# Kernel tuning notes

Hardware: AMD Instinct MI355X
Metric: run time of the kernel (lower is better)

## Reference

```python
import collections
import functools
import itertools
import math
import jax
import jax.numpy as jnp
import numpy as np

# Weight space: RNN-like {W_ih:(784,512), W_hh:(512,512), b:(512,)}, channels last.
N0, N1, C_IN, C_OUT = 784, 512, 16, 16
PERM_SPEC = [[0, 1], [1, 1], [1]]  # perm-group label per dim of each leaf
N_TERMS = [11, 25, 9]  # equivariant basis terms per output leaf (Bell-number products)


def diagonal_slice(X, matching_dims):
    out = jnp.diagonal(X, axis1=matching_dims[0], axis2=matching_dims[1])
    for dim in matching_dims[2:]:
        out = jnp.diagonal(out, axis1=dim, axis2=-1)
    return out


def find_missing_indices(lstA, lstB):
    setB = set(lstB)
    return [i for i, el in enumerate(lstA) if el not in setB]


def get_repeated_idcs(lst):
    index_map = {}
    for index, item in enumerate(lst):
        index_map.setdefault(item, []).append(index)
    return [idcs for idcs in index_map.values() if len(idcs) > 1]


def match_dim_order(X, X_idcs, out_idcs):
    X_idcs_copy = X_idcs[:]
    perm = []
    for idx in out_idcs:
        if idx in X_idcs_copy:
            i = X_idcs_copy.index(idx)
            perm.append(i)
            X_idcs_copy[i] = None
    X = jnp.transpose(X, perm)
    return X, [X_idcs[i] for i in perm]


def remove_idcs(lst, idcs):
    return [l for i, l in enumerate(lst) if i not in idcs]


def move_dims_to_end(X, dims):
    new_in_order = remove_idcs(list(range(X.ndim)), dims) + dims
    return jnp.transpose(X, new_in_order)


def generate_partitions(items):
    if len(items) == 1:
        yield [items]
        return
    first = items[0]
    for subpart in generate_partitions(items[1:]):
        for n, subset in enumerate(subpart):
            yield subpart[:n] + [[first] + subset] + subpart[n + 1:]
        yield [[first]] + subpart


def valid_partitions(indices, perms):
    groups = collections.defaultdict(list)
    for index, perm in zip(indices, perms):
        groups[perm].append(index)
    parts_per_group = [list(generate_partitions(g)) for g in groups.values()]
    for p in itertools.product(*parts_per_group):
        yield [s for s in itertools.chain(*p)]


def gen_terms(out_spec, in_spec, out_shape, inp):
    """Basis terms of an equivariant linear map from in_spec to out_spec."""
    terms = []
    k1, k2 = len(out_spec), len(in_spec)
    for partition in valid_partitions(list(range(k1 + k2)), list(out_spec) + list(in_spec)):
        indices = [-1] * (k1 + k2)
        for subset_idx, subset in enumerate(partition):
            for dim in subset:
                indices[dim] = subset_idx
        out_indices, in_indices = indices[:k1], indices[k1:]
        term = inp
        # Collapse repeated input indices via diagonals.
        while (rep_idcs := get_repeated_idcs(in_indices)):
            term = diagonal_slice(term, rep_idcs[0])
            idx = in_indices[rep_idcs[0][0]]
            in_indices = remove_idcs(in_indices, rep_idcs[0])
            in_indices.append(idx)
        # Mean-reduce input dims that do not appear in the output.
        agg_idcs = find_missing_indices(in_indices, out_indices)
        term = jnp.mean(term, axis=agg_idcs)
        in_indices = remove_idcs(in_indices, agg_idcs)
        # Scatter onto diagonals for repeated output indices.
        for diag_set in get_repeated_idcs(out_indices):
            dim_size, out_idx = out_shape[diag_set[0]], out_indices[diag_set[0]]
            matching_in_dims = [i for i, idx in enumerate(in_indices) if idx == out_idx]
            num_new_dims = len(diag_set) - len(matching_in_dims)
            term = move_dims_to_end(term, matching_in_dims)
            new_term = jnp.zeros(term.shape + (dim_size,) * num_new_dims, dtype=term.dtype)
            diag_slice = (jnp.s_[:],) * (new_term.ndim - len(diag_set)) + (jnp.arange(dim_size),) * len(diag_set)
            if not matching_in_dims:
                term = jnp.expand_dims(term, axis=-1)
            term = new_term.at[diag_slice].add(term)
            in_indices = remove_idcs(in_indices, matching_in_dims)
            in_indices.extend([out_idx] * len(diag_set))
        term, in_indices = match_dim_order(term, in_indices, out_indices)
        term = jnp.expand_dims(term, axis=find_missing_indices(out_indices, in_indices))
        terms.append(term)
    return terms


def setup_inputs() -> dict:
    key = jax.random.key(0)
    ks = jax.random.split(key, 6)
    inp = {
        "w_ih": jax.random.normal(ks[0], (N0, N1, C_IN), jnp.float32),
        "w_hh": jax.random.normal(ks[1], (N1, N1, C_IN), jnp.float32),
        "b": jax.random.normal(ks[2], (N1, C_IN), jnp.float32),
    }
    for i, n in enumerate(N_TERMS):
        scale = math.sqrt(2.0 / (C_IN * n))  # 'he' init, fan_in = c_in * n_terms
        inp[f"theta_{i}"] = scale * jax.random.normal(ks[3 + i], (n, C_IN, C_OUT), jnp.float32)
        inp[f"bias_{i}"] = jnp.zeros((C_OUT,), jnp.float32)
    return inp


def reference(w_ih, w_hh, b, theta_0, theta_1, theta_2, bias_0, bias_1, bias_2):
    flat_params = [w_ih, w_hh, b]
    thetas = [theta_0, theta_1, theta_2]
    biases = [bias_0, bias_1, bias_2]
    outs = []
    for i in range(3):
        terms_i = []
        for j in range(3):
            gen = jax.vmap(
                functools.partial(gen_terms, PERM_SPEC[i], PERM_SPEC[j], flat_params[i].shape),
                in_axes=-1, out_axes=-1)
            terms_i.extend(gen(flat_params[j]))
        out = biases[i]
        for k, term in enumerate(terms_i):
            out = out + term @ thetas[i][k]  # [..., c_in] @ [c_in, c_out]
        outs.append(out)
    return tuple(outs)
```

## Files before the change

### kernel.cpp

```cpp
#include <hip/hip_runtime.h>


#define N0 784
#define N1 512

__device__ __forceinline__ float4 f4add(float4 a, float4 b) {
  a.x += b.x; a.y += b.y; a.z += b.z; a.w += b.w; return a;
}

__global__ __launch_bounds__(256)
void k_stage1(const float* __restrict__ wih, const float* __restrict__ whh,
              float* __restrict__ rm_ih, float* __restrict__ cm_ih,
              float* __restrict__ rm_hh, float* __restrict__ cm_hh,
              float* __restrict__ d_hh) {
  __shared__ float4 red[256];
  int t = threadIdx.x, blk = blockIdx.x;
  float4 acc = make_float4(0.f, 0.f, 0.f, 0.f);
  float scale;
  float* dst;
  if (blk < N0) {
    const float4* row = (const float4*)(wih + (size_t)blk * 8192);
    for (int j = t; j < 2048; j += 256) acc = f4add(acc, row[j]);
    scale = 1.f / 512.f; dst = rm_ih + blk * 16;
  } else if (blk < N0 + N1) {
    int b = blk - N0, q = t & 3, g = t >> 2;
    for (int a = g; a < N0; a += 64)
      acc = f4add(acc, *(const float4*)(wih + (size_t)a * 8192 + b * 16 + q * 4));
    scale = 1.f / 784.f; dst = cm_ih + b * 16;
  } else if (blk < N0 + 2 * N1) {
    int b = blk - N0 - N1;
    const float4* row = (const float4*)(whh + (size_t)b * 8192);
    for (int j = t; j < 2048; j += 256) acc = f4add(acc, row[j]);
    scale = 1.f / 512.f; dst = rm_hh + b * 16;
  } else {
    int b = blk - N0 - 2 * N1, q = t & 3, g = t >> 2;
    for (int a = g; a < N1; a += 64)
      acc = f4add(acc, *(const float4*)(whh + (size_t)a * 8192 + b * 16 + q * 4));
    scale = 1.f / 512.f; dst = cm_hh + b * 16;
    if (t < 4) ((float4*)(d_hh + b * 16))[t] = *(const float4*)(whh + (size_t)b * 8192 + b * 16 + t * 4);
  }
  red[t] = acc; __syncthreads();
  #pragma unroll
  for (int s = 128; s >= 4; s >>= 1) {
    if (t < s) red[t] = f4add(red[t], red[t + s]);
    __syncthreads();
  }
  if (t < 4) {
    float4 m = red[t];
    ((float4*)dst)[t] = make_float4(m.x * scale, m.y * scale, m.z * scale, m.w * scale);
  }
}

__global__ __launch_bounds__(256)
void k_vec(const float* __restrict__ rm_ih, const float* __restrict__ cm_ih,
           const float* __restrict__ rm_hh, const float* __restrict__ cm_hh,
           const float* __restrict__ d_hh, const float* __restrict__ bvec,
           const float* __restrict__ th0, const float* __restrict__ bias0,
           const float* __restrict__ th1, const float* __restrict__ bias1,
           const float* __restrict__ th2, const float* __restrict__ bias2,
           float* __restrict__ A0C, float* __restrict__ B0,
           float* __restrict__ A1C, float* __restrict__ B1,
           float* __restrict__ DD1, float* __restrict__ out2) {
  __shared__ float th[11520];
  __shared__ float4 red[256];
  __shared__ float gv[4][16];
  __shared__ float sc[64];
  int t = threadIdx.x;
  {
    float4* t4 = (float4*)th;
    const float4* s0 = (const float4*)th0;
    const float4* s1 = (const float4*)th1;
    const float4* s2 = (const float4*)th2;
    for (int j = t; j < 704; j += 256) t4[j] = s0[j];
    for (int j = t; j < 1600; j += 256) t4[704 + j] = s1[j];
    for (int j = t; j < 576; j += 256) t4[2304 + j] = s2[j];
  }
  int q = t & 3, g = t >> 2;
  {
    float4 acc = make_float4(0.f, 0.f, 0.f, 0.f);
    for (int a = g; a < N0; a += 64) acc = f4add(acc, ((const float4*)rm_ih)[a * 4 + q]);
    red[t] = acc; __syncthreads();
    #pragma unroll
    for (int s = 128; s >= 4; s >>= 1) { if (t < s) red[t] = f4add(red[t], red[t + s]); __syncthreads(); }
    if (t < 4) {
      float4 m = red[t];
      gv[0][t * 4 + 0] = m.x / 784.f; gv[0][t * 4 + 1] = m.y / 784.f;
      gv[0][t * 4 + 2] = m.z / 784.f; gv[0][t * 4 + 3] = m.w / 784.f;
    }
    __syncthreads();
  }
  const float* srcs[3] = { d_hh, rm_hh, bvec };
  #pragma unroll
  for (int v = 0; v < 3; v++) {
    float4 acc = make_float4(0.f, 0.f, 0.f, 0.f);
    for (int a = g; a < N1; a += 64) acc = f4add(acc, ((const float4*)srcs[v])[a * 4 + q]);
    red[t] = acc; __syncthreads();
    #pragma unroll
    for (int s = 128; s >= 4; s >>= 1) { if (t < s) red[t] = f4add(red[t], red[t + s]); __syncthreads(); }
    if (t < 4) {
      float4 m = red[t];
      gv[v + 1][t * 4 + 0] = m.x / 512.f; gv[v + 1][t * 4 + 1] = m.y / 512.f;
      gv[v + 1][t * 4 + 2] = m.z / 512.f; gv[v + 1][t * 4 + 3] = m.w / 512.f;
    }
    __syncthreads();
  }
  {
    int co = t & 15, j = t >> 4, o = j * 16 + co;
    float g0v = gv[0][j], dm = gv[1][j], gh = gv[2][j], mv = gv[3][j];
    float4 p;
    p.x = g0v * th[768 + o]         + dm * th[1280 + o]        + gh * th[2048 + o]        + mv * th[2560 + o];
    p.y = g0v * th[2816 + 1024 + o] + dm * th[2816 + 2304 + o] + gh * th[2816 + 4864 + o] + mv * th[2816 + 6144 + o];
    p.z = g0v * th[2816 + 512 + o]  + dm * th[2816 + 1792 + o] + gh * th[2816 + 4096 + o] + mv * th[2816 + 5632 + o];
    p.w = g0v * th[9216 + 256 + o]  + dm * th[9216 + 768 + o]  + gh * th[9216 + 1536 + o] + mv * th[9216 + 2048 + o];
    red[t] = p; __syncthreads();
    #pragma unroll
    for (int s = 128; s >= 16; s >>= 1) { if (t < s) red[t] = f4add(red[t], red[t + s]); __syncthreads(); }
    if (t < 16) {
      float4 a = red[t];
      sc[t] = a.x + bias0[t];
      sc[16 + t] = a.y + bias1[t];
      sc[32 + t] = a.z;
      sc[48 + t] = a.w + bias2[t];
    }
    __syncthreads();
  }
  int idx = blockIdx.x * 256 + t;
  int i = idx >> 4, co = idx & 15;
  float a0 = sc[co];
  {
    const float4* r4 = (const float4*)(rm_ih + i * 16);
    #pragma unroll
    for (int kq = 0; kq < 4; kq++) {
      float4 r = r4[kq];
      float vr[4] = { r.x, r.y, r.z, r.w };
      #pragma unroll
      for (int e = 0; e < 4; e++) a0 += vr[e] * th[256 + (kq * 4 + e) * 16 + co];
    }
  }
  A0C[idx] = a0;
  if (i < N1) {
    float b0a = 0.f, a1 = sc[16 + co], b1a = 0.f, dd = sc[32 + co], o2 = sc[48 + co];
    const float4* c4 = (const float4*)(cm_ih + i * 16);
    const float4* d4 = (const float4*)(d_hh + i * 16);
    const float4* r4 = (const float4*)(rm_hh + i * 16);
    const float4* m4 = (const float4*)(cm_hh + i * 16);
    const float4* v4 = (const float4*)(bvec + i * 16);
    #pragma unroll
    for (int kq = 0; kq < 4; kq++) {
      float4 cq = c4[kq], dq = d4[kq], rq = r4[kq], mq = m4[kq], vq = v4[kq];
      float vc[4] = { cq.x, cq.y, cq.z, cq.w };
      float vd[4] = { dq.x, dq.y, dq.z, dq.w };
      float vr[4] = { rq.x, rq.y, rq.z, rq.w };
      float vm[4] = { mq.x, mq.y, mq.z, mq.w };
      float vb[4] = { vq.x, vq.y, vq.z, vq.w };
      #pragma unroll
      for (int e = 0; e < 4; e++) {
        int o = (kq * 4 + e) * 16 + co;
        float cmi = vc[e], d = vd[e], r = vr[e], cm = vm[e], v = vb[e];
        b0a += cmi * th[512 + o]         + d * th[1024 + o]        + r * th[1536 + o]        + cm * th[1792 + o]        + v * th[2304 + o];
        a1  += cmi * th[2816 + 768 + o]  + d * th[2816 + 2048 + o] + r * th[2816 + 4352 + o] + cm * th[2816 + 4608 + o] + v * th[2816 + 5888 + o];
        b1a += cmi * th[2816 + 256 + o]  + d * th[2816 + 1536 + o] + r * th[2816 + 3072 + o] + cm * th[2816 + 3840 + o] + v * th[2816 + 5376 + o];
        dd  += cmi * th[2816 + 0 + o]    + d * th[2816 + 1280 + o] + r * th[2816 + 2560 + o] + cm * th[2816 + 3584 + o] + v * th[2816 + 5120 + o];
        o2  += cmi * th[9216 + 0 + o]    + d * th[9216 + 512 + o]  + r * th[9216 + 1024 + o] + cm * th[9216 + 1280 + o] + v * th[9216 + 1792 + o];
      }
    }
    B0[idx] = b0a; A1C[idx] = a1; B1[idx] = b1a; DD1[idx] = dd; out2[idx] = o2;
  }
}

__global__ __launch_bounds__(256)
void k_out(const float* __restrict__ wih, const float* __restrict__ whh,
           const float* __restrict__ th0, const float* __restrict__ th1,
           const float* __restrict__ A0C, const float* __restrict__ B0,
           const float* __restrict__ A1C, const float* __restrict__ B1,
           const float* __restrict__ DD1,
           float* __restrict__ out0, float* __restrict__ out1) {
  if (blockIdx.x < 1024) {
    int tid = blockIdx.x * 256 + threadIdx.x;
    int q = tid & 3;
    int slot = tid >> 2;
    const int nslots = (1024 * 256) >> 2;
    float4 tq[16];
    #pragma unroll
    for (int k = 0; k < 16; k++) tq[k] = *(const float4*)(th0 + k * 16 + q * 4);
    for (int p = slot; p < N0 * N1; p += nslots) {
      const float4* row = (const float4*)(wih + (size_t)p * 16);
      float4 r0 = row[0], r1 = row[1], r2 = row[2], r3 = row[3];
      int a = p >> 9, bb = p & 511;
      float4 acc = *(const float4*)(A0C + a * 16 + q * 4);
      float4 b4 = *(const float4*)(B0 + bb * 16 + q * 4);
      acc.x += b4.x; acc.y += b4.y; acc.z += b4.z; acc.w += b4.w;
      float wv[16] = { r0.x, r0.y, r0.z, r0.w, r1.x, r1.y, r1.z, r1.w,
                       r2.x, r2.y, r2.z, r2.w, r3.x, r3.y, r3.z, r3.w };
      #pragma unroll
      for (int k = 0; k < 16; k++) {
        acc.x += wv[k] * tq[k].x; acc.y += wv[k] * tq[k].y;
        acc.z += wv[k] * tq[k].z; acc.w += wv[k] * tq[k].w;
      }
      *(float4*)(out0 + (size_t)p * 16 + q * 4) = acc;
    }
  } else {
    int tid = (blockIdx.x - 1024) * 256 + threadIdx.x;
    int q = tid & 7;
    int slot = tid >> 3;
    const int nslots = (1024 * 256) >> 3;
    float2 tA[16], tB[16];
    #pragma unroll
    for (int k = 0; k < 16; k++) {
      tA[k] = *(const float2*)(th1 + 13 * 256 + k * 16 + q * 2);
      tB[k] = *(const float2*)(th1 + 11 * 256 + k * 16 + q * 2);
    }
    for (int p = slot; p < N1 * N1; p += nslots) {
      int a = p >> 9, b = p & 511;
      const float4* ra = (const float4*)(whh + (size_t)p * 16);
      const float4* rt = (const float4*)(whh + (size_t)((b << 9) | a) * 16);
      float4 a0 = ra[0], a1v = ra[1], a2 = ra[2], a3 = ra[3];
      float4 t0 = rt[0], t1v = rt[1], t2 = rt[2], t3 = rt[3];
      float2 acc = *(const float2*)(A1C + a * 16 + q * 2);
      float2 bb = *(const float2*)(B1 + b * 16 + q * 2);
      acc.x += bb.x; acc.y += bb.y;
      if (a == b) {
        float2 dd = *(const float2*)(DD1 + a * 16 + q * 2);
        acc.x += dd.x; acc.y += dd.y;
      }
      float ya[16] = { a0.x, a0.y, a0.z, a0.w, a1v.x, a1v.y, a1v.z, a1v.w,
                       a2.x, a2.y, a2.z, a2.w, a3.x, a3.y, a3.z, a3.w };
      float yt[16] = { t0.x, t0.y, t0.z, t0.w, t1v.x, t1v.y, t1v.z, t1v.w,
                       t2.x, t2.y, t2.z, t2.w, t3.x, t3.y, t3.z, t3.w };
      #pragma unroll
      for (int k = 0; k < 16; k++) {
        acc.x += ya[k] * tA[k].x + yt[k] * tB[k].x;
        acc.y += ya[k] * tA[k].y + yt[k] * tB[k].y;
      }
      *(float2*)(out1 + (size_t)p * 16 + q * 2) = acc;
    }
  }
}

extern "C" void kernel_launch(void* const* d_in, const int* in_sizes, int n_in,
                              void* d_out, int out_size, void* d_ws, size_t ws_size,
                              hipStream_t stream) {
  const float* w_ih = (const float*)d_in[0];
  const float* w_hh = (const float*)d_in[1];
  const float* bvec = (const float*)d_in[2];
  const float *th0, *bias0, *th1, *bias1, *th2, *bias2;
  if (n_in >= 9 && in_sizes[4] == 16) {
    th0 = (const float*)d_in[3]; bias0 = (const float*)d_in[4];
    th1 = (const float*)d_in[5]; bias1 = (const float*)d_in[6];
    th2 = (const float*)d_in[7]; bias2 = (const float*)d_in[8];
  } else {
    th0 = (const float*)d_in[3]; th1 = (const float*)d_in[4]; th2 = (const float*)d_in[5];
    bias0 = (const float*)d_in[6]; bias1 = (const float*)d_in[7]; bias2 = (const float*)d_in[8];
  }
  float* ws    = (float*)d_ws;
  float* rm_ih = ws;
  float* cm_ih = rm_ih + 12544;
  float* rm_hh = cm_ih + 8192;
  float* cm_hh = rm_hh + 8192;
  float* d_hh  = cm_hh + 8192;
  float* A0C   = d_hh + 8192;
  float* B0    = A0C + 12544;
  float* A1C   = B0 + 8192;
  float* B1    = A1C + 8192;
  float* DD1   = B1 + 8192;
  float* out0 = (float*)d_out;
  float* out1 = out0 + (size_t)N0 * N1 * 16;
  float* out2 = out1 + (size_t)N1 * N1 * 16;

  hipLaunchKernelGGL(k_stage1, dim3(N0 + 3 * N1), dim3(256), 0, stream,
                     w_ih, w_hh, rm_ih, cm_ih, rm_hh, cm_hh, d_hh);
  hipLaunchKernelGGL(k_vec, dim3(49), dim3(256), 0, stream,
                     rm_ih, cm_ih, rm_hh, cm_hh, d_hh, bvec,
                     th0, bias0, th1, bias1, th2, bias2,
                     A0C, B0, A1C, B1, DD1, out2);
  hipLaunchKernelGGL(k_out, dim3(2048), dim3(256), 0, stream,
                     w_ih, w_hh, th0, th1, A0C, B0, A1C, B1, DD1, out0, out1);
}
```

Baseline: 153.6 us.

## Compute row and column means in one pass with per-block column partials

Stage 1 previously read each weight matrix twice: once per row for row means and once with strided column reads for column means. Now each block reads 4 rows once, accumulating row sums and per-block column partial sums in shared memory, and writes the partials to workspace. k_vec then reduces those partials to get the column means. This halves the stage-1 reads of the large weights, at the cost of extra partial writes and a serial 196/128-step reduction loop inside the small 49-block k_vec.

```diff
diff --git a/kernel.cpp b/kernel.cpp
--- a/kernel.cpp
+++ b/kernel.cpp
@@ -3,6 +3,9 @@
 
 #define N0 784
 #define N1 512
+#define RPB 4
+#define NB_IH (N0 / RPB)
+#define NB_HH (N1 / RPB)
 
 __device__ __forceinline__ float4 f4add(float4 a, float4 b) {
   a.x += b.x; a.y += b.y; a.z += b.z; a.w += b.w; return a;
@@ -10,51 +13,58 @@
 
 __global__ __launch_bounds__(256)
 void k_stage1(const float* __restrict__ wih, const float* __restrict__ whh,
-              float* __restrict__ rm_ih, float* __restrict__ cm_ih,
-              float* __restrict__ rm_hh, float* __restrict__ cm_hh,
-              float* __restrict__ d_hh) {
-  __shared__ float4 red[256];
+              float* __restrict__ rm_ih, float* __restrict__ rm_hh,
+              float* __restrict__ d_hh,
+              float* __restrict__ part_ih, float* __restrict__ part_hh) {
+  __shared__ float4 colacc[2048];
+  __shared__ float4 redAll[RPB][256];
   int t = threadIdx.x, blk = blockIdx.x;
-  float4 acc = make_float4(0.f, 0.f, 0.f, 0.f);
-  float scale;
-  float* dst;
-  if (blk < N0) {
-    const float4* row = (const float4*)(wih + (size_t)blk * 8192);
-    for (int j = t; j < 2048; j += 256) acc = f4add(acc, row[j]);
-    scale = 1.f / 512.f; dst = rm_ih + blk * 16;
-  } else if (blk < N0 + N1) {
-    int b = blk - N0, q = t & 3, g = t >> 2;
-    for (int a = g; a < N0; a += 64)
-      acc = f4add(acc, *(const float4*)(wih + (size_t)a * 8192 + b * 16 + q * 4));
-    scale = 1.f / 784.f; dst = cm_ih + b * 16;
-  } else if (blk < N0 + 2 * N1) {
-    int b = blk - N0 - N1;
-    const float4* row = (const float4*)(whh + (size_t)b * 8192);
-    for (int j = t; j < 2048; j += 256) acc = f4add(acc, row[j]);
-    scale = 1.f / 512.f; dst = rm_hh + b * 16;
-  } else {
-    int b = blk - N0 - 2 * N1, q = t & 3, g = t >> 2;
-    for (int a = g; a < N1; a += 64)
-      acc = f4add(acc, *(const float4*)(whh + (size_t)a * 8192 + b * 16 + q * 4));
-    scale = 1.f / 512.f; dst = cm_hh + b * 16;
-    if (t < 4) ((float4*)(d_hh + b * 16))[t] = *(const float4*)(whh + (size_t)b * 8192 + b * 16 + t * 4);
-  }
-  red[t] = acc; __syncthreads();
+  bool is_hh = blk >= NB_IH;
+  const float* W = is_hh ? whh : wih;
+  float* rm      = is_hh ? rm_hh : rm_ih;
+  float* part    = is_hh ? part_hh : part_ih;
+  int pblk = is_hh ? blk - NB_IH : blk;
+  int r0 = pblk * RPB;
+
+  for (int j = t; j < 2048; j += 256) colacc[j] = make_float4(0.f, 0.f, 0.f, 0.f);
+  #pragma unroll
+  for (int r = 0; r < RPB; r++) {
+    const float4* row = (const float4*)(W + (size_t)(r0 + r) * 8192);
+    float4 acc = make_float4(0.f, 0.f, 0.f, 0.f);
+    for (int j = t; j < 2048; j += 256) {
+      float4 v = row[j];
+      colacc[j] = f4add(colacc[j], v);
+      acc = f4add(acc, v);
+    }
+    redAll[r][t] = acc;
+  }
+  __syncthreads();
   #pragma unroll
   for (int s = 128; s >= 4; s >>= 1) {
-    if (t < s) red[t] = f4add(red[t], red[t + s]);
+    if (t < s) {
+      #pragma unroll
+      for (int r = 0; r < RPB; r++) redAll[r][t] = f4add(redAll[r][t], redAll[r][t + s]);
+    }
     __syncthreads();
   }
-  if (t < 4) {
-    float4 m = red[t];
-    ((float4*)dst)[t] = make_float4(m.x * scale, m.y * scale, m.z * scale, m.w * scale);
-  }
+  if (t < 16) {
+    int r = t >> 2, q = t & 3;
+    float4 m = redAll[r][q];
+    const float s = 1.f / 512.f;
+    ((float4*)(rm + (r0 + r) * 16))[q] = make_float4(m.x * s, m.y * s, m.z * s, m.w * s);
+  }
+  if (is_hh && t < 64) {
+    int r = t >> 4, ci = t & 15;
+    d_hh[(r0 + r) * 16 + ci] = whh[(size_t)(r0 + r) * 8192 + (r0 + r) * 16 + ci];
+  }
+  float4* p4 = (float4*)(part + (size_t)pblk * 8192);
+  for (int j = t; j < 2048; j += 256) p4[j] = colacc[j];
 }
 
 __global__ __launch_bounds__(256)
-void k_vec(const float* __restrict__ rm_ih, const float* __restrict__ cm_ih,
-           const float* __restrict__ rm_hh, const float* __restrict__ cm_hh,
+void k_vec(const float* __restrict__ rm_ih, const float* __restrict__ rm_hh,
            const float* __restrict__ d_hh, const float* __restrict__ bvec,
+           const float* __restrict__ part_ih, const float* __restrict__ part_hh,
            const float* __restrict__ th0, const float* __restrict__ bias0,
            const float* __restrict__ th1, const float* __restrict__ bias1,
            const float* __restrict__ th2, const float* __restrict__ bias2,
@@ -65,6 +75,8 @@
   __shared__ float4 red[256];
   __shared__ float gv[4][16];
   __shared__ float sc[64];
+  __shared__ float cmih_s[16][16];
+  __shared__ float cmhh_s[16][16];
   int t = threadIdx.x;
   {
     float4* t4 = (float4*)th;
@@ -75,6 +87,19 @@
     for (int j = t; j < 1600; j += 256) t4[704 + j] = s1[j];
     for (int j = t; j < 576; j += 256) t4[2304 + j] = s2[j];
   }
+  int il = t >> 4, co = t & 15;
+  int i0 = blockIdx.x * 16;
+  if (i0 < N1) {
+    int col = i0 + il;
+    float s1 = 0.f;
+    #pragma unroll 4
+    for (int p = 0; p < NB_IH; p++) s1 += part_ih[(size_t)p * 8192 + col * 16 + co];
+    cmih_s[il][co] = s1 * (1.f / 784.f);
+    float s2 = 0.f;
+    #pragma unroll 4
+    for (int p = 0; p < NB_HH; p++) s2 += part_hh[(size_t)p * 8192 + col * 16 + co];
+    cmhh_s[il][co] = s2 * (1.f / 512.f);
+  }
   int q = t & 3, g = t >> 2;
   {
     float4 acc = make_float4(0.f, 0.f, 0.f, 0.f);
@@ -105,7 +130,7 @@
     __syncthreads();
   }
   {
-    int co = t & 15, j = t >> 4, o = j * 16 + co;
+    int j = t >> 4, o = j * 16 + co;
     float g0v = gv[0][j], dm = gv[1][j], gh = gv[2][j], mv = gv[3][j];
     float4 p;
     p.x = g0v * th[768 + o]         + dm * th[1280 + o]        + gh * th[2048 + o]        + mv * th[2560 + o];
@@ -125,7 +150,7 @@
     __syncthreads();
   }
   int idx = blockIdx.x * 256 + t;
-  int i = idx >> 4, co = idx & 15;
+  int i = i0 + il;
   float a0 = sc[co];
   {
     const float4* r4 = (const float4*)(rm_ih + i * 16);
@@ -140,23 +165,21 @@
   A0C[idx] = a0;
   if (i < N1) {
     float b0a = 0.f, a1 = sc[16 + co], b1a = 0.f, dd = sc[32 + co], o2 = sc[48 + co];
-    const float4* c4 = (const float4*)(cm_ih + i * 16);
     const float4* d4 = (const float4*)(d_hh + i * 16);
     const float4* r4 = (const float4*)(rm_hh + i * 16);
-    const float4* m4 = (const float4*)(cm_hh + i * 16);
     const float4* v4 = (const float4*)(bvec + i * 16);
     #pragma unroll
     for (int kq = 0; kq < 4; kq++) {
-      float4 cq = c4[kq], dq = d4[kq], rq = r4[kq], mq = m4[kq], vq = v4[kq];
-      float vc[4] = { cq.x, cq.y, cq.z, cq.w };
+      float4 dq = d4[kq], rq = r4[kq], vq = v4[kq];
       float vd[4] = { dq.x, dq.y, dq.z, dq.w };
       float vr[4] = { rq.x, rq.y, rq.z, rq.w };
-      float vm[4] = { mq.x, mq.y, mq.z, mq.w };
       float vb[4] = { vq.x, vq.y, vq.z, vq.w };
       #pragma unroll
       for (int e = 0; e < 4; e++) {
-        int o = (kq * 4 + e) * 16 + co;
-        float cmi = vc[e], d = vd[e], r = vr[e], cm = vm[e], v = vb[e];
+        int k = kq * 4 + e;
+        int o = k * 16 + co;
+        float cmi = cmih_s[il][k], cm = cmhh_s[il][k];
+        float d = vd[e], r = vr[e], v = vb[e];
         b0a += cmi * th[512 + o]         + d * th[1024 + o]        + r * th[1536 + o]        + cm * th[1792 + o]        + v * th[2304 + o];
         a1  += cmi * th[2816 + 768 + o]  + d * th[2816 + 2048 + o] + r * th[2816 + 4352 + o] + cm * th[2816 + 4608 + o] + v * th[2816 + 5888 + o];
         b1a += cmi * th[2816 + 256 + o]  + d * th[2816 + 1536 + o] + r * th[2816 + 3072 + o] + cm * th[2816 + 3840 + o] + v * th[2816 + 5376 + o];
@@ -252,25 +275,25 @@
     th0 = (const float*)d_in[3]; th1 = (const float*)d_in[4]; th2 = (const float*)d_in[5];
     bias0 = (const float*)d_in[6]; bias1 = (const float*)d_in[7]; bias2 = (const float*)d_in[8];
   }
-  float* ws    = (float*)d_ws;
-  float* rm_ih = ws;
-  float* cm_ih = rm_ih + 12544;
-  float* rm_hh = cm_ih + 8192;
-  float* cm_hh = rm_hh + 8192;
-  float* d_hh  = cm_hh + 8192;
-  float* A0C   = d_hh + 8192;
-  float* B0    = A0C + 12544;
-  float* A1C   = B0 + 8192;
-  float* B1    = A1C + 8192;
-  float* DD1   = B1 + 8192;
+  float* ws      = (float*)d_ws;
+  float* rm_ih   = ws;
+  float* rm_hh   = rm_ih + 12544;
+  float* d_hh    = rm_hh + 8192;
+  float* A0C     = d_hh + 8192;
+  float* B0      = A0C + 12544;
+  float* A1C     = B0 + 8192;
+  float* B1      = A1C + 8192;
+  float* DD1     = B1 + 8192;
+  float* part_ih = DD1 + 8192;
+  float* part_hh = part_ih + NB_IH * 8192;
   float* out0 = (float*)d_out;
   float* out1 = out0 + (size_t)N0 * N1 * 16;
   float* out2 = out1 + (size_t)N1 * N1 * 16;
 
-  hipLaunchKernelGGL(k_stage1, dim3(N0 + 3 * N1), dim3(256), 0, stream,
-                     w_ih, w_hh, rm_ih, cm_ih, rm_hh, cm_hh, d_hh);
+  hipLaunchKernelGGL(k_stage1, dim3(NB_IH + NB_HH), dim3(256), 0, stream,
+                     w_ih, w_hh, rm_ih, rm_hh, d_hh, part_ih, part_hh);
   hipLaunchKernelGGL(k_vec, dim3(49), dim3(256), 0, stream,
-                     rm_ih, cm_ih, rm_hh, cm_hh, d_hh, bvec,
+                     rm_ih, rm_hh, d_hh, bvec, part_ih, part_hh,
                      th0, bias0, th1, bias1, th2, bias2,
                      A0C, B0, A1C, B1, DD1, out2);
   hipLaunchKernelGGL(k_out, dim3(2048), dim3(256), 0, stream,
```

New measurement: 170.8 us. +11.2%, slower.

## Hoist global means into a separate kernel and use nontemporal output stores

Applied to the files above, without the earlier changes.

The four global mean reductions move out of each of the 49 k_vec blocks into a new 4-block kernel, so they are no longer recomputed redundantly per block. The per-block scalar-coefficient reduction becomes a per-thread 16-step loop. The large output writes in k_out now use nontemporal stores to reduce cache pollution on a streaming write. This adds one more kernel launch and a small global buffer.

```diff
diff --git a/kernel.cpp b/kernel.cpp
--- a/kernel.cpp
+++ b/kernel.cpp
@@ -4,8 +4,19 @@
 #define N0 784
 #define N1 512
 
+typedef float v4f __attribute__((ext_vector_type(4)));
+typedef float v2f __attribute__((ext_vector_type(2)));
+
 __device__ __forceinline__ float4 f4add(float4 a, float4 b) {
   a.x += b.x; a.y += b.y; a.z += b.z; a.w += b.w; return a;
+}
+__device__ __forceinline__ void nt_store4(float* p, float4 v) {
+  v4f x; x[0] = v.x; x[1] = v.y; x[2] = v.z; x[3] = v.w;
+  __builtin_nontemporal_store(x, (v4f*)p);
+}
+__device__ __forceinline__ void nt_store2(float* p, float x0, float x1) {
+  v2f x; x[0] = x0; x[1] = x1;
+  __builtin_nontemporal_store(x, (v2f*)p);
 }
 
 __global__ __launch_bounds__(256)
@@ -52,9 +63,38 @@
 }
 
 __global__ __launch_bounds__(256)
+void k_small(const float* __restrict__ rm_ih, const float* __restrict__ d_hh,
+             const float* __restrict__ rm_hh, const float* __restrict__ bvec,
+             float* __restrict__ gv_g) {
+  __shared__ float4 red[256];
+  int t = threadIdx.x, q = t & 3, g = t >> 2;
+  const float* src; int n; float scale;
+  switch (blockIdx.x) {
+    case 0: src = rm_ih; n = N0; scale = 1.f / 784.f; break;
+    case 1: src = d_hh;  n = N1; scale = 1.f / 512.f; break;
+    case 2: src = rm_hh; n = N1; scale = 1.f / 512.f; break;
+    default: src = bvec; n = N1; scale = 1.f / 512.f; break;
+  }
+  float4 acc = make_float4(0.f, 0.f, 0.f, 0.f);
+  for (int a = g; a < n; a += 64) acc = f4add(acc, ((const float4*)src)[a * 4 + q]);
+  red[t] = acc; __syncthreads();
+  #pragma unroll
+  for (int s = 128; s >= 4; s >>= 1) {
+    if (t < s) red[t] = f4add(red[t], red[t + s]);
+    __syncthreads();
+  }
+  if (t < 4) {
+    float4 m = red[t];
+    float* dst = gv_g + blockIdx.x * 16 + t * 4;
+    dst[0] = m.x * scale; dst[1] = m.y * scale; dst[2] = m.z * scale; dst[3] = m.w * scale;
+  }
+}
+
+__global__ __launch_bounds__(256)
 void k_vec(const float* __restrict__ rm_ih, const float* __restrict__ cm_ih,
            const float* __restrict__ rm_hh, const float* __restrict__ cm_hh,
            const float* __restrict__ d_hh, const float* __restrict__ bvec,
+           const float* __restrict__ gv_g,
            const float* __restrict__ th0, const float* __restrict__ bias0,
            const float* __restrict__ th1, const float* __restrict__ bias1,
            const float* __restrict__ th2, const float* __restrict__ bias2,
@@ -62,9 +102,7 @@
            float* __restrict__ A1C, float* __restrict__ B1,
            float* __restrict__ DD1, float* __restrict__ out2) {
   __shared__ float th[11520];
-  __shared__ float4 red[256];
-  __shared__ float gv[4][16];
-  __shared__ float sc[64];
+  __shared__ float gvs[64];
   int t = threadIdx.x;
   {
     float4* t4 = (float4*)th;
@@ -74,59 +112,23 @@
     for (int j = t; j < 704; j += 256) t4[j] = s0[j];
     for (int j = t; j < 1600; j += 256) t4[704 + j] = s1[j];
     for (int j = t; j < 576; j += 256) t4[2304 + j] = s2[j];
-  }
-  int q = t & 3, g = t >> 2;
-  {
-    float4 acc = make_float4(0.f, 0.f, 0.f, 0.f);
-    for (int a = g; a < N0; a += 64) acc = f4add(acc, ((const float4*)rm_ih)[a * 4 + q]);
-    red[t] = acc; __syncthreads();
-    #pragma unroll
-    for (int s = 128; s >= 4; s >>= 1) { if (t < s) red[t] = f4add(red[t], red[t + s]); __syncthreads(); }
-    if (t < 4) {
-      float4 m = red[t];
-      gv[0][t * 4 + 0] = m.x / 784.f; gv[0][t * 4 + 1] = m.y / 784.f;
-      gv[0][t * 4 + 2] = m.z / 784.f; gv[0][t * 4 + 3] = m.w / 784.f;
-    }
-    __syncthreads();
-  }
-  const float* srcs[3] = { d_hh, rm_hh, bvec };
+    if (t < 64) gvs[t] = gv_g[t];
+  }
+  __syncthreads();
+  int co = t & 15;
+  float c0 = bias0[co], c1 = bias1[co], e1 = 0.f, s2v = bias2[co];
   #pragma unroll
-  for (int v = 0; v < 3; v++) {
-    float4 acc = make_float4(0.f, 0.f, 0.f, 0.f);
-    for (int a = g; a < N1; a += 64) acc = f4add(acc, ((const float4*)srcs[v])[a * 4 + q]);
-    red[t] = acc; __syncthreads();
-    #pragma unroll
-    for (int s = 128; s >= 4; s >>= 1) { if (t < s) red[t] = f4add(red[t], red[t + s]); __syncthreads(); }
-    if (t < 4) {
-      float4 m = red[t];
-      gv[v + 1][t * 4 + 0] = m.x / 512.f; gv[v + 1][t * 4 + 1] = m.y / 512.f;
-      gv[v + 1][t * 4 + 2] = m.z / 512.f; gv[v + 1][t * 4 + 3] = m.w / 512.f;
-    }
-    __syncthreads();
-  }
-  {
-    int co = t & 15, j = t >> 4, o = j * 16 + co;
-    float g0v = gv[0][j], dm = gv[1][j], gh = gv[2][j], mv = gv[3][j];
-    float4 p;
-    p.x = g0v * th[768 + o]         + dm * th[1280 + o]        + gh * th[2048 + o]        + mv * th[2560 + o];
-    p.y = g0v * th[2816 + 1024 + o] + dm * th[2816 + 2304 + o] + gh * th[2816 + 4864 + o] + mv * th[2816 + 6144 + o];
-    p.z = g0v * th[2816 + 512 + o]  + dm * th[2816 + 1792 + o] + gh * th[2816 + 4096 + o] + mv * th[2816 + 5632 + o];
-    p.w = g0v * th[9216 + 256 + o]  + dm * th[9216 + 768 + o]  + gh * th[9216 + 1536 + o] + mv * th[9216 + 2048 + o];
-    red[t] = p; __syncthreads();
-    #pragma unroll
-    for (int s = 128; s >= 16; s >>= 1) { if (t < s) red[t] = f4add(red[t], red[t + s]); __syncthreads(); }
-    if (t < 16) {
-      float4 a = red[t];
-      sc[t] = a.x + bias0[t];
-      sc[16 + t] = a.y + bias1[t];
-      sc[32 + t] = a.z;
-      sc[48 + t] = a.w + bias2[t];
-    }
-    __syncthreads();
+  for (int j = 0; j < 16; j++) {
+    int o = j * 16 + co;
+    float g0v = gvs[j], dm = gvs[16 + j], gh = gvs[32 + j], mv = gvs[48 + j];
+    c0  += g0v * th[768 + o]         + dm * th[1280 + o]        + gh * th[2048 + o]        + mv * th[2560 + o];
+    c1  += g0v * th[2816 + 1024 + o] + dm * th[2816 + 2304 + o] + gh * th[2816 + 4864 + o] + mv * th[2816 + 6144 + o];
+    e1  += g0v * th[2816 + 512 + o]  + dm * th[2816 + 1792 + o] + gh * th[2816 + 4096 + o] + mv * th[2816 + 5632 + o];
+    s2v += g0v * th[9216 + 256 + o]  + dm * th[9216 + 768 + o]  + gh * th[9216 + 1536 + o] + mv * th[9216 + 2048 + o];
   }
   int idx = blockIdx.x * 256 + t;
-  int i = idx >> 4, co = idx & 15;
-  float a0 = sc[co];
+  int i = idx >> 4;
+  float a0 = c0;
   {
     const float4* r4 = (const float4*)(rm_ih + i * 16);
     #pragma unroll
@@ -139,7 +141,7 @@
   }
   A0C[idx] = a0;
   if (i < N1) {
-    float b0a = 0.f, a1 = sc[16 + co], b1a = 0.f, dd = sc[32 + co], o2 = sc[48 + co];
+    float b0a = 0.f, a1 = c1, b1a = 0.f, dd = e1, o2 = s2v;
     const float4* c4 = (const float4*)(cm_ih + i * 16);
     const float4* d4 = (const float4*)(d_hh + i * 16);
     const float4* r4 = (const float4*)(rm_hh + i * 16);
@@ -197,7 +199,7 @@
         acc.x += wv[k] * tq[k].x; acc.y += wv[k] * tq[k].y;
         acc.z += wv[k] * tq[k].z; acc.w += wv[k] * tq[k].w;
       }
-      *(float4*)(out0 + (size_t)p * 16 + q * 4) = acc;
+      nt_store4(out0 + (size_t)p * 16 + q * 4, acc);
     }
   } else {
     int tid = (blockIdx.x - 1024) * 256 + threadIdx.x;
@@ -232,7 +234,7 @@
         acc.x += ya[k] * tA[k].x + yt[k] * tB[k].x;
         acc.y += ya[k] * tA[k].y + yt[k] * tB[k].y;
       }
-      *(float2*)(out1 + (size_t)p * 16 + q * 2) = acc;
+      nt_store2(out1 + (size_t)p * 16 + q * 2, acc.x, acc.y);
     }
   }
 }
@@ -263,14 +265,17 @@
   float* A1C   = B0 + 8192;
   float* B1    = A1C + 8192;
   float* DD1   = B1 + 8192;
+  float* gv_g  = DD1 + 8192;
   float* out0 = (float*)d_out;
   float* out1 = out0 + (size_t)N0 * N1 * 16;
   float* out2 = out1 + (size_t)N1 * N1 * 16;
 
   hipLaunchKernelGGL(k_stage1, dim3(N0 + 3 * N1), dim3(256), 0, stream,
                      w_ih, w_hh, rm_ih, cm_ih, rm_hh, cm_hh, d_hh);
+  hipLaunchKernelGGL(k_small, dim3(4), dim3(256), 0, stream,
+                     rm_ih, d_hh, rm_hh, bvec, gv_g);
   hipLaunchKernelGGL(k_vec, dim3(49), dim3(256), 0, stream,
-                     rm_ih, cm_ih, rm_hh, cm_hh, d_hh, bvec,
+                     rm_ih, cm_ih, rm_hh, cm_hh, d_hh, bvec, gv_g,
                      th0, bias0, th1, bias1, th2, bias2,
                      A0C, B0, A1C, B1, DD1, out2);
   hipLaunchKernelGGL(k_out, dim3(2048), dim3(256), 0, stream,
```

Measured after the change: 150.4 us. -2.1%, faster.
